# Kernel optimization log

Hardware: AMD Instinct MI355X
Metric: run time of the kernel (lower is better)

The kernel has to match this reference:

```python
import jax, jax.numpy as jnp
import numpy as np

N = 20000        # nodes
E = 320000       # edges
F_IN = 512       # feature_size
H = 512          # hidden_dim (z dim)
OUT = 1024       # output_size


def setup_inputs() -> dict:
    key = jax.random.key(0)
    ks = jax.random.split(key, 24)
    p = lambda k, shape: jax.random.normal(k, shape, jnp.float32) * 0.02
    return {
        "x": jax.random.normal(ks[0], (N, F_IN), jnp.float32),
        "edge_index": jax.random.randint(ks[1], (2, E), 0, N),
        "edge_weight": jax.random.uniform(ks[2], (E,), dtype=jnp.float32),
        "beta": jnp.float32(1.0),
        "y_target": jax.random.uniform(ks[3], (1,), dtype=jnp.float32),
        "eps": jax.random.normal(ks[4], (N, H), jnp.float32),
        # GCNConv weights (in_dim, out_dim) + bias
        "W1": p(ks[5], (F_IN, 1024)), "b1": jnp.zeros((1024,), jnp.float32),
        "W2": p(ks[6], (1024, 512)), "b2": jnp.zeros((512,), jnp.float32),
        "W3": p(ks[7], (512, 256)),  "b3": jnp.zeros((256,), jnp.float32),
        # VAE heads
        "Wmu": p(ks[8], (256, H)),  "bmu": jnp.zeros((H,), jnp.float32),
        "Wlv": p(ks[9], (256, H)),  "blv": jnp.zeros((H,), jnp.float32),
        # decoder MLP: (2H+1) -> (2H+1) -> OUT
        "Wd1": p(ks[10], (2 * H + 1, 2 * H + 1)), "bd1": jnp.zeros((2 * H + 1,), jnp.float32),
        "Wd2": p(ks[11], (2 * H + 1, OUT)),       "bd2": jnp.zeros((OUT,), jnp.float32),
    }


def gcn_conv(x, W, b, src, dst, ew):
    # PyG GCNConv: add self-loops (weight 1), symmetric deg normalization,
    # aggregate normalized neighbor messages of x @ W, then add bias.
    xw = x @ W                                             # [N, out]
    deg = jax.ops.segment_sum(ew, dst, num_segments=N) + 1.0
    dinv = jax.lax.rsqrt(deg)                              # [N]
    norm = dinv[src] * ew * dinv[dst]                      # [E]
    agg = jax.ops.segment_sum(norm[:, None] * xw[src], dst, num_segments=N)
    return agg + (dinv * dinv)[:, None] * xw + b


def l2norm(x):
    n = jnp.sqrt(jnp.sum(x * x, axis=1, keepdims=True))
    return x / jnp.maximum(n, 1e-12)


def reference(x, edge_index, edge_weight, beta, y_target, eps,
              W1, b1, W2, b2, W3, b3, Wmu, bmu, Wlv, blv, Wd1, bd1, Wd2, bd2):
    src, dst = edge_index[0], edge_index[1]
    h = jax.nn.relu(l2norm(gcn_conv(x, W1, b1, src, dst, edge_weight)))
    h = jax.nn.relu(l2norm(gcn_conv(h, W2, b2, src, dst, edge_weight)))
    h = jax.nn.relu(l2norm(gcn_conv(h, W3, b3, src, dst, edge_weight)))
    mu = h @ Wmu + bmu                                     # [N, H]
    logvar = h @ Wlv + blv                                 # [N, H]
    # reparameterize(mu, beta * logvar) with eps ~ 0.01 * N(0,1)
    std = jnp.exp(0.5 * beta * logvar)
    z = mu + (0.01 * eps) * std                            # [N, H]
    out1 = jnp.max(z, axis=0, keepdims=True)               # global max pool [1, H]
    out2 = jnp.mean(z, axis=0, keepdims=True)              # global mean pool [1, H]
    reduce_z = jnp.concatenate([out1, out2, y_target[:, None]], axis=-1)  # [1, 2H+1]
    hdec = jax.nn.relu(reduce_z @ Wd1 + bd1)
    recon_x = jax.nn.sigmoid(hdec @ Wd2 + bd2)             # [1, OUT]
    return (recon_x, mu, logvar)
```

## Files before the change

kernel.cpp:

```cpp
#include <hip/hip_runtime.h>

#define NN 20000
#define EE 320000
#define RCH 40
#define RPC 500
#define MPAD 20096
#define DKB 128
#define DCH 9

typedef unsigned short u16;
typedef unsigned int u32;
typedef __attribute__((ext_vector_type(8))) short short8;
typedef __attribute__((ext_vector_type(4))) float f32x4;

__device__ inline float bf16lo(u32 u) { return __uint_as_float(u << 16); }
__device__ inline float bf16hi(u32 u) { return __uint_as_float(u & 0xffff0000u); }
__device__ inline u16 f2b(float f) {
  u32 u = __float_as_uint(f);
  u += 0x7fffu + ((u >> 16) & 1u);
  return (u16)(u >> 16);
}
__device__ inline u32 pack2(float a, float b) {
  return (u32)f2b(a) | ((u32)f2b(b) << 16);
}

__device__ inline void gload16(const void* g, void* l) {
  __builtin_amdgcn_global_load_lds(
      (const __attribute__((address_space(1))) void*)g,
      (__attribute__((address_space(3))) void*)l, 16, 0, 0);
}

__global__ void k_zeroi(int* __restrict__ p, int n) {
  int i = blockIdx.x * blockDim.x + threadIdx.x;
  if (i < n) p[i] = 0;
}

__global__ void k_f2b2(const float* __restrict__ in, u16* __restrict__ out, int npairs) {
  for (int i = blockIdx.x * blockDim.x + threadIdx.x; i < npairs; i += gridDim.x * blockDim.x) {
    float2 v = *(const float2*)(in + 2 * i);
    ((u32*)out)[i] = pack2(v.x, v.y);
  }
}

__global__ void k_wt(const float* __restrict__ W, u16* __restrict__ WT, int K, int N) {
  int k = blockIdx.y * 256 + threadIdx.x;
  int n = blockIdx.x;
  WT[(size_t)n * K + k] = f2b(W[(size_t)k * N + n]);
}

__global__ void k_count(const int* __restrict__ ei, int* __restrict__ counts) {
  int e = blockIdx.x * blockDim.x + threadIdx.x;
  if (e < EE) atomicAdd(counts + ei[EE + e], 1);
}

__global__ __launch_bounds__(256)
void k_scan(const int* __restrict__ counts, int* __restrict__ rowptr, int* __restrict__ cursor) {
  const int CHUNK = (NN + 255) / 256;
  int t = threadIdx.x;
  int lo = t * CHUNK, hi = min(lo + CHUNK, NN);
  int s = 0;
  for (int i = lo; i < hi; ++i) s += counts[i];
  __shared__ int tsum[256];
  tsum[t] = s;
  __syncthreads();
  if (t == 0) {
    int run = 0;
    for (int i = 0; i < 256; ++i) { int v = tsum[i]; tsum[i] = run; run += v; }
  }
  __syncthreads();
  int run = tsum[t];
  for (int i = lo; i < hi; ++i) {
    rowptr[i] = run;
    cursor[i] = run;
    run += counts[i];
  }
  if (t == 255) rowptr[NN] = EE;
}

__global__ void k_fill(const int* __restrict__ ei, const float* __restrict__ ew,
                       int* __restrict__ cursor, int* __restrict__ colsrc,
                       float* __restrict__ ecw) {
  int e = blockIdx.x * blockDim.x + threadIdx.x;
  if (e < EE) {
    int d = ei[EE + e];
    int pos = atomicAdd(cursor + d, 1);
    colsrc[pos] = ei[e];
    ecw[pos] = ew[e];
  }
}

__global__ void k_degcsr(const int* __restrict__ rowptr, const float* __restrict__ ecw,
                         float* __restrict__ dinv, float* __restrict__ dinv2) {
  int i = blockIdx.x * blockDim.x + threadIdx.x;
  if (i < NN) {
    float s = 0.f;
    for (int e = rowptr[i]; e < rowptr[i + 1]; ++e) s += ecw[e];
    float d = s + 1.0f;
    dinv[i] = rsqrtf(d);
    dinv2[i] = 1.0f / d;
  }
}

template <bool STORE_BF16, bool HAS_BIAS>
__global__ __launch_bounds__(256)
void k_mfma(const u16* __restrict__ A, const u16* __restrict__ BT,
            const float* __restrict__ bias, void* __restrict__ C,
            int M, int K, int N) {
  __shared__ u16 Asm[128 * 32];
  __shared__ u16 Bsm[128 * 32];
  const int tid = threadIdx.x;
  const int m0 = blockIdx.x * 128;
  const int n0 = blockIdx.y * 128;
  const int lane = tid & 63;
  const int wave = tid >> 6;
  const int wm = (wave >> 1) * 64;
  const int wn = (wave & 1) * 64;
  const int qm = lane & 15;
  const int quad = lane >> 4;

  f32x4 acc[4][4];
#pragma unroll
  for (int i = 0; i < 4; ++i)
#pragma unroll
    for (int j = 0; j < 4; ++j) acc[i][j] = (f32x4){0.f, 0.f, 0.f, 0.f};

  for (int k0 = 0; k0 < K; k0 += 32) {
#pragma unroll
    for (int h = 0; h < 2; ++h) {
      int c = h * 256 + tid;
      int row = c >> 2, kc = c & 3;
      gload16(A + (size_t)(m0 + row) * K + k0 + kc * 8, Asm + c * 8);
      gload16(BT + (size_t)(n0 + row) * K + k0 + kc * 8, Bsm + c * 8);
    }
    __syncthreads();
    short8 af[4], bfr[4];
#pragma unroll
    for (int i = 0; i < 4; ++i)
      af[i] = *(const short8*)(Asm + (wm + i * 16 + qm) * 32 + quad * 8);
#pragma unroll
    for (int j = 0; j < 4; ++j)
      bfr[j] = *(const short8*)(Bsm + (wn + j * 16 + qm) * 32 + quad * 8);
#pragma unroll
    for (int i = 0; i < 4; ++i)
#pragma unroll
      for (int j = 0; j < 4; ++j)
        acc[i][j] = __builtin_amdgcn_mfma_f32_16x16x32_bf16(af[i], bfr[j], acc[i][j], 0, 0, 0);
    __syncthreads();
  }

#pragma unroll
  for (int i = 0; i < 4; ++i) {
#pragma unroll
    for (int r = 0; r < 4; ++r) {
      int row = m0 + wm + i * 16 + quad * 4 + r;
      if (row >= M) continue;
#pragma unroll
      for (int j = 0; j < 4; ++j) {
        int col = n0 + wn + j * 16 + qm;
        float v = acc[i][j][r];
        if (HAS_BIAS) v += bias[col];
        if (STORE_BF16) ((u16*)C)[(size_t)row * N + col] = f2b(v);
        else ((float*)C)[(size_t)row * N + col] = v;
      }
    }
  }
}

template <int NT, bool PRE>
__global__ __launch_bounds__(NT)
void k_gather(const int* __restrict__ rowptr, const int* __restrict__ colsrc,
              const float* __restrict__ ecw, const float* __restrict__ dinv,
              const float* __restrict__ dinv2, const u16* __restrict__ xw,
              const float* __restrict__ bias, u16* __restrict__ h) {
  const int O = 2 * NT;
  const int row = blockIdx.x;
  const int tid = threadIdx.x;
  const float dv = dinv[row], dv2 = dinv2[row];
  u32 u = ((const u32*)(xw + (size_t)row * O))[tid];
  float a0 = dv2 * bf16lo(u);
  float a1 = dv2 * bf16hi(u);
  if (!PRE) { a0 += bias[2 * tid]; a1 += bias[2 * tid + 1]; }

  __shared__ int s_src[NT];
  __shared__ float s_w[NT];
  const int e0 = rowptr[row], e1 = rowptr[row + 1];
  for (int base = e0; base < e1; base += NT) {
    int cnt = min(NT, e1 - base);
    __syncthreads();
    if (tid < cnt) {
      int s = colsrc[base + tid];
      s_src[tid] = s;
      s_w[tid] = dinv[s] * ecw[base + tid] * dv;
    }
    __syncthreads();
    for (int e = 0; e < cnt; ++e) {
      float w = s_w[e];
      u32 v = ((const u32*)(xw + (size_t)s_src[e] * O))[tid];
      a0 += w * bf16lo(v);
      a1 += w * bf16hi(v);
    }
  }

  if (PRE) {
    ((u32*)h)[(size_t)row * NT + tid] = pack2(a0, a1);
    return;
  }
  float ss = a0 * a0 + a1 * a1;
#pragma unroll
  for (int off = 32; off > 0; off >>= 1) ss += __shfl_down(ss, off, 64);
  __shared__ float red[NT / 64];
  __shared__ float s_scale;
  if ((tid & 63) == 0) red[tid >> 6] = ss;
  __syncthreads();
  if (tid == 0) {
    float t = 0.f;
#pragma unroll
    for (int i = 0; i < NT / 64; ++i) t += red[i];
    s_scale = 1.0f / fmaxf(sqrtf(t), 1e-12f);
  }
  __syncthreads();
  float sc = s_scale;
  ((u32*)h)[(size_t)row * NT + tid] = pack2(fmaxf(a0 * sc, 0.f), fmaxf(a1 * sc, 0.f));
}

__global__ __launch_bounds__(256)
void k_l2relu(const u16* __restrict__ t, u16* __restrict__ h) {
  const int row = blockIdx.x;
  const int tid = threadIdx.x;
  const u32* tr = (const u32*)(t + (size_t)row * 1024);
  u32 u0 = tr[tid], u1 = tr[256 + tid];
  float a0 = bf16lo(u0), a1 = bf16hi(u0), a2 = bf16lo(u1), a3 = bf16hi(u1);
  float ss = a0 * a0 + a1 * a1 + a2 * a2 + a3 * a3;
#pragma unroll
  for (int off = 32; off > 0; off >>= 1) ss += __shfl_down(ss, off, 64);
  __shared__ float red[4];
  __shared__ float s_scale;
  if ((tid & 63) == 0) red[tid >> 6] = ss;
  __syncthreads();
  if (tid == 0) {
    float s = red[0] + red[1] + red[2] + red[3];
    s_scale = 1.0f / fmaxf(sqrtf(s), 1e-12f);
  }
  __syncthreads();
  float sc = s_scale;
  u32* hr = (u32*)(h + (size_t)row * 1024);
  hr[tid]       = pack2(fmaxf(a0 * sc, 0.f), fmaxf(a1 * sc, 0.f));
  hr[256 + tid] = pack2(fmaxf(a2 * sc, 0.f), fmaxf(a3 * sc, 0.f));
}

__global__ void k_pool_partial(const float* __restrict__ mu, const float* __restrict__ lv,
                               const float* __restrict__ eps, const float* __restrict__ beta_p,
                               float* __restrict__ pmax, float* __restrict__ psum) {
  int tx = threadIdx.x, ty = threadIdx.y;
  int col = blockIdx.x * 64 + tx;
  int by = blockIdx.y;
  float beta = beta_p[0];
  float m = -3.4e38f, s = 0.f;
  for (int i = by * RPC + ty; i < (by + 1) * RPC; i += 4) {
    size_t idx = (size_t)i * 512 + col;
    float z = mu[idx] + 0.01f * eps[idx] * expf(0.5f * beta * lv[idx]);
    m = fmaxf(m, z);
    s += z;
  }
  __shared__ float sm[4][64], su[4][64];
  sm[ty][tx] = m; su[ty][tx] = s;
  __syncthreads();
  if (ty == 0) {
    m = fmaxf(fmaxf(sm[0][tx], sm[1][tx]), fmaxf(sm[2][tx], sm[3][tx]));
    s = su[0][tx] + su[1][tx] + su[2][tx] + su[3][tx];
    pmax[(size_t)by * 512 + col] = m;
    psum[(size_t)by * 512 + col] = s;
  }
}

__global__ void k_pool_combine(const float* __restrict__ pmax, const float* __restrict__ psum,
                               const float* __restrict__ yt, float* __restrict__ rz) {
  int col = threadIdx.x;
  float m = -3.4e38f, s = 0.f;
  for (int c = 0; c < RCH; ++c) {
    m = fmaxf(m, pmax[(size_t)c * 512 + col]);
    s += psum[(size_t)c * 512 + col];
  }
  rz[col] = m;
  rz[512 + col] = s / (float)NN;
  if (col == 0) rz[1024] = yt[0];
}

__global__ __launch_bounds__(256)
void k_dec_partial(const float* __restrict__ v, const float* __restrict__ W,
                   float* __restrict__ partial, int Kdim, int Ndim) {
  int b = blockIdx.x;
  int lo = b * DCH;
  float rv[DCH];
#pragma unroll
  for (int j = 0; j < DCH; ++j) rv[j] = (lo + j < Kdim) ? v[lo + j] : 0.f;
  for (int n = threadIdx.x; n < Ndim; n += 256) {
    float s = 0.f;
#pragma unroll
    for (int j = 0; j < DCH; ++j)
      if (lo + j < Kdim) s += rv[j] * W[(size_t)(lo + j) * Ndim + n];
    partial[(size_t)b * Ndim + n] = s;
  }
}

template <int ACT>
__global__ __launch_bounds__(256)
void k_dec_combine(const float* __restrict__ partial, const float* __restrict__ bias,
                   float* __restrict__ out, int Ndim) {
  int n = blockIdx.x * 256 + threadIdx.x;
  if (n >= Ndim) return;
  float s = bias[n];
  for (int b = 0; b < DKB; ++b) s += partial[(size_t)b * Ndim + n];
  out[n] = (ACT == 0) ? fmaxf(s, 0.f) : 1.0f / (1.0f + expf(-s));
}

extern "C" void kernel_launch(void* const* d_in, const int* in_sizes, int n_in,
                              void* d_out, int out_size, void* d_ws, size_t ws_size,
                              hipStream_t stream) {
  const float* x    = (const float*)d_in[0];
  const int*   ei   = (const int*)d_in[1];
  const float* ew   = (const float*)d_in[2];
  const float* beta = (const float*)d_in[3];
  const float* yt   = (const float*)d_in[4];
  const float* eps  = (const float*)d_in[5];
  const float* W1   = (const float*)d_in[6];  const float* b1  = (const float*)d_in[7];
  const float* W2   = (const float*)d_in[8];  const float* b2  = (const float*)d_in[9];
  const float* W3   = (const float*)d_in[10]; const float* b3  = (const float*)d_in[11];
  const float* Wmu  = (const float*)d_in[12]; const float* bmu = (const float*)d_in[13];
  const float* Wlv  = (const float*)d_in[14]; const float* blv = (const float*)d_in[15];
  const float* Wd1  = (const float*)d_in[16]; const float* bd1 = (const float*)d_in[17];
  const float* Wd2  = (const float*)d_in[18]; const float* bd2 = (const float*)d_in[19];

  char* wsb = (char*)d_ws;
  size_t off = 0;
  auto alloc_f = [&](size_t n) { float* p = (float*)(wsb + off); off += n * sizeof(float); return p; };
  auto alloc_i = [&](size_t n) { int* p = (int*)(wsb + off); off += n * sizeof(int); return p; };
  auto alloc_h = [&](size_t n) { u16* p = (u16*)(wsb + off); off += ((n * 2 + 3) & ~(size_t)3); return p; };

  int* counts  = alloc_i(NN);
  int* rowptr  = alloc_i(NN + 1);
  int* cursor  = alloc_i(NN);
  int* colsrc  = alloc_i(EE);
  float* ecw   = alloc_f(EE);
  float* dinv  = alloc_f(NN);
  float* din2  = alloc_f(NN);
  float* pmax  = alloc_f(RCH * 512);
  float* psum  = alloc_f(RCH * 512);
  float* rz    = alloc_f(1028);
  float* hdec  = alloc_f(1028);
  float* part1 = alloc_f((size_t)DKB * 1025);
  float* part2 = alloc_f((size_t)DKB * 1024);
  u16* W1T  = alloc_h(1024 * 512);
  u16* W2T  = alloc_h(512 * 1024);
  u16* W3T  = alloc_h(256 * 512);
  u16* WmuT = alloc_h(512 * 256);
  u16* WlvT = alloc_h(512 * 256);
  u16* xb   = alloc_h((size_t)MPAD * 512);
  u16* aggx = alloc_h((size_t)MPAD * 512);
  u16* bufT = alloc_h((size_t)MPAD * 1024);
  u16* bufH = alloc_h((size_t)MPAD * 1024);
  u16* h2   = alloc_h((size_t)MPAD * 512);
  u16* h3   = xb;
  u16* z2   = bufT;
  u16* z3   = bufH;

  float* out_f  = (float*)d_out;
  float* mu_out = out_f + 1024;
  float* lv_out = out_f + 1024 + (size_t)NN * 512;

  const int MT = (NN + 127) / 128;

  k_f2b2<<<4096, 256, 0, stream>>>(x, xb, NN * 512 / 2);
  k_wt<<<dim3(1024, 2), 256, 0, stream>>>(W1, W1T, 512, 1024);
  k_wt<<<dim3(512, 4), 256, 0, stream>>>(W2, W2T, 1024, 512);
  k_wt<<<dim3(256, 2), 256, 0, stream>>>(W3, W3T, 512, 256);
  k_wt<<<dim3(512, 1), 256, 0, stream>>>(Wmu, WmuT, 256, 512);
  k_wt<<<dim3(512, 1), 256, 0, stream>>>(Wlv, WlvT, 256, 512);

  k_zeroi<<<(NN + 255) / 256, 256, 0, stream>>>(counts, NN);
  k_count<<<(EE + 255) / 256, 256, 0, stream>>>(ei, counts);
  k_scan<<<1, 256, 0, stream>>>(counts, rowptr, cursor);
  k_fill<<<(EE + 255) / 256, 256, 0, stream>>>(ei, ew, cursor, colsrc, ecw);
  k_degcsr<<<(NN + 255) / 256, 256, 0, stream>>>(rowptr, ecw, dinv, din2);

  k_gather<256, true><<<NN, 256, 0, stream>>>(rowptr, colsrc, ecw, dinv, din2, xb, nullptr, aggx);
  k_mfma<true, true><<<dim3(MT, 8), 256, 0, stream>>>(aggx, W1T, b1, bufT, NN, 512, 1024);
  k_l2relu<<<NN, 256, 0, stream>>>(bufT, bufH);

  k_mfma<true, false><<<dim3(MT, 4), 256, 0, stream>>>(bufH, W2T, nullptr, z2, NN, 1024, 512);
  k_gather<256, false><<<NN, 256, 0, stream>>>(rowptr, colsrc, ecw, dinv, din2, z2, b2, h2);

  k_mfma<true, false><<<dim3(MT, 2), 256, 0, stream>>>(h2, W3T, nullptr, z3, NN, 512, 256);
  k_gather<128, false><<<NN, 128, 0, stream>>>(rowptr, colsrc, ecw, dinv, din2, z3, b3, h3);

  k_mfma<false, true><<<dim3(MT, 4), 256, 0, stream>>>(h3, WmuT, bmu, mu_out, NN, 256, 512);
  k_mfma<false, true><<<dim3(MT, 4), 256, 0, stream>>>(h3, WlvT, blv, lv_out, NN, 256, 512);

  k_pool_partial<<<dim3(8, RCH), dim3(64, 4), 0, stream>>>(mu_out, lv_out, eps, beta, pmax, psum);
  k_pool_combine<<<1, 512, 0, stream>>>(pmax, psum, yt, rz);

  k_dec_partial<<<DKB, 256, 0, stream>>>(rz, Wd1, part1, 1025, 1025);
  k_dec_combine<0><<<5, 256, 0, stream>>>(part1, bd1, hdec, 1025);
  k_dec_partial<<<DKB, 256, 0, stream>>>(hdec, Wd2, part2, 1025, 1024);
  k_dec_combine<1><<<4, 256, 0, stream>>>(part2, bd2, out_f, 1024);
}
```

Baseline: 732.4 us.

## Fuse mu/logvar head GEMMs with reparameterization and pooling partials

Replaces the two separate head GEMMs and the pooling partial kernel with one kernel that computes mu and logvar for the same tile, then the reparameterized z and per-tile column max and sum in the epilogue. This avoids re-reading the 2x20000x512 float outputs for pooling and shares the A-tile loads between both heads. The cost is double the accumulator registers (128 floats per thread), which may reduce occupancy, and a combine step over 157 tile partials instead of 40.

```diff
diff --git a/kernel.cpp b/kernel.cpp
--- a/kernel.cpp
+++ b/kernel.cpp
@@ -2,9 +2,8 @@
 
 #define NN 20000
 #define EE 320000
-#define RCH 40
-#define RPC 500
 #define MPAD 20096
+#define MTILES 157
 #define DKB 128
 #define DCH 9
 
@@ -166,6 +165,136 @@
   }
 }
 
+__global__ __launch_bounds__(256)
+void k_heads(const u16* __restrict__ A, const u16* __restrict__ BmuT,
+             const u16* __restrict__ BlvT, const float* __restrict__ bmu,
+             const float* __restrict__ blv, const float* __restrict__ eps,
+             const float* __restrict__ beta_p, float* __restrict__ mu_out,
+             float* __restrict__ lv_out, float* __restrict__ pmax,
+             float* __restrict__ psum) {
+  const int K = 256, N = 512;
+  __shared__ u16 Asm[128 * 32];
+  __shared__ u16 Bmu[128 * 32];
+  __shared__ u16 Blv[128 * 32];
+  __shared__ float smax[256], ssum[256];
+  const int tid = threadIdx.x;
+  const int m0 = blockIdx.x * 128;
+  const int n0 = blockIdx.y * 128;
+  const int lane = tid & 63;
+  const int wave = tid >> 6;
+  const int wm = (wave >> 1) * 64;
+  const int wn = (wave & 1) * 64;
+  const int qm = lane & 15;
+  const int quad = lane >> 4;
+
+  f32x4 am[4][4], al[4][4];
+#pragma unroll
+  for (int i = 0; i < 4; ++i)
+#pragma unroll
+    for (int j = 0; j < 4; ++j) {
+      am[i][j] = (f32x4){0.f, 0.f, 0.f, 0.f};
+      al[i][j] = (f32x4){0.f, 0.f, 0.f, 0.f};
+    }
+
+  for (int k0 = 0; k0 < K; k0 += 32) {
+#pragma unroll
+    for (int h = 0; h < 2; ++h) {
+      int c = h * 256 + tid;
+      int row = c >> 2, kc = c & 3;
+      gload16(A + (size_t)(m0 + row) * K + k0 + kc * 8, Asm + c * 8);
+      gload16(BmuT + (size_t)(n0 + row) * K + k0 + kc * 8, Bmu + c * 8);
+      gload16(BlvT + (size_t)(n0 + row) * K + k0 + kc * 8, Blv + c * 8);
+    }
+    __syncthreads();
+    short8 af[4], bm[4], bl[4];
+#pragma unroll
+    for (int i = 0; i < 4; ++i)
+      af[i] = *(const short8*)(Asm + (wm + i * 16 + qm) * 32 + quad * 8);
+#pragma unroll
+    for (int j = 0; j < 4; ++j) {
+      bm[j] = *(const short8*)(Bmu + (wn + j * 16 + qm) * 32 + quad * 8);
+      bl[j] = *(const short8*)(Blv + (wn + j * 16 + qm) * 32 + quad * 8);
+    }
+#pragma unroll
+    for (int i = 0; i < 4; ++i)
+#pragma unroll
+      for (int j = 0; j < 4; ++j) {
+        am[i][j] = __builtin_amdgcn_mfma_f32_16x16x32_bf16(af[i], bm[j], am[i][j], 0, 0, 0);
+        al[i][j] = __builtin_amdgcn_mfma_f32_16x16x32_bf16(af[i], bl[j], al[i][j], 0, 0, 0);
+      }
+    __syncthreads();
+  }
+
+  const float beta = beta_p[0];
+  float biasm[4], biasl[4];
+#pragma unroll
+  for (int j = 0; j < 4; ++j) {
+    int col = n0 + wn + j * 16 + qm;
+    biasm[j] = bmu[col];
+    biasl[j] = blv[col];
+  }
+  float zmax[4] = {-3.4e38f, -3.4e38f, -3.4e38f, -3.4e38f};
+  float zsum[4] = {0.f, 0.f, 0.f, 0.f};
+#pragma unroll
+  for (int i = 0; i < 4; ++i) {
+#pragma unroll
+    for (int r = 0; r < 4; ++r) {
+      int row = m0 + wm + i * 16 + quad * 4 + r;
+      if (row >= NN) continue;
+#pragma unroll
+      for (int j = 0; j < 4; ++j) {
+        int col = n0 + wn + j * 16 + qm;
+        float vm = am[i][j][r] + biasm[j];
+        float vl = al[i][j][r] + biasl[j];
+        size_t idx = (size_t)row * N + col;
+        mu_out[idx] = vm;
+        lv_out[idx] = vl;
+        float z = vm + 0.01f * eps[idx] * expf(0.5f * beta * vl);
+        zmax[j] = fmaxf(zmax[j], z);
+        zsum[j] += z;
+      }
+    }
+  }
+#pragma unroll
+  for (int j = 0; j < 4; ++j) {
+#pragma unroll
+    for (int off = 16; off <= 32; off <<= 1) {
+      zmax[j] = fmaxf(zmax[j], __shfl_xor(zmax[j], off, 64));
+      zsum[j] += __shfl_xor(zsum[j], off, 64);
+    }
+  }
+  if (quad == 0) {
+#pragma unroll
+    for (int j = 0; j < 4; ++j) {
+      smax[wave * 64 + j * 16 + qm] = zmax[j];
+      ssum[wave * 64 + j * 16 + qm] = zsum[j];
+    }
+  }
+  __syncthreads();
+  if (tid < 128) {
+    int cn = tid;
+    int w0 = (cn < 64) ? 0 : 1;
+    int c = cn & 63;
+    float m = fmaxf(smax[w0 * 64 + c], smax[(w0 + 2) * 64 + c]);
+    float s = ssum[w0 * 64 + c] + ssum[(w0 + 2) * 64 + c];
+    pmax[(size_t)blockIdx.x * N + n0 + cn] = m;
+    psum[(size_t)blockIdx.x * N + n0 + cn] = s;
+  }
+}
+
+__global__ void k_zred(const float* __restrict__ pmax, const float* __restrict__ psum,
+                       const float* __restrict__ yt, float* __restrict__ rz) {
+  int col = threadIdx.x;
+  float m = -3.4e38f, s = 0.f;
+  for (int c = 0; c < MTILES; ++c) {
+    m = fmaxf(m, pmax[(size_t)c * 512 + col]);
+    s += psum[(size_t)c * 512 + col];
+  }
+  rz[col] = m;
+  rz[512 + col] = s / (float)NN;
+  if (col == 0) rz[1024] = yt[0];
+}
+
 template <int NT, bool PRE>
 __global__ __launch_bounds__(NT)
 void k_gather(const int* __restrict__ rowptr, const int* __restrict__ colsrc,
@@ -246,44 +375,6 @@
   u32* hr = (u32*)(h + (size_t)row * 1024);
   hr[tid]       = pack2(fmaxf(a0 * sc, 0.f), fmaxf(a1 * sc, 0.f));
   hr[256 + tid] = pack2(fmaxf(a2 * sc, 0.f), fmaxf(a3 * sc, 0.f));
-}
-
-__global__ void k_pool_partial(const float* __restrict__ mu, const float* __restrict__ lv,
-                               const float* __restrict__ eps, const float* __restrict__ beta_p,
-                               float* __restrict__ pmax, float* __restrict__ psum) {
-  int tx = threadIdx.x, ty = threadIdx.y;
-  int col = blockIdx.x * 64 + tx;
-  int by = blockIdx.y;
-  float beta = beta_p[0];
-  float m = -3.4e38f, s = 0.f;
-  for (int i = by * RPC + ty; i < (by + 1) * RPC; i += 4) {
-    size_t idx = (size_t)i * 512 + col;
-    float z = mu[idx] + 0.01f * eps[idx] * expf(0.5f * beta * lv[idx]);
-    m = fmaxf(m, z);
-    s += z;
-  }
-  __shared__ float sm[4][64], su[4][64];
-  sm[ty][tx] = m; su[ty][tx] = s;
-  __syncthreads();
-  if (ty == 0) {
-    m = fmaxf(fmaxf(sm[0][tx], sm[1][tx]), fmaxf(sm[2][tx], sm[3][tx]));
-    s = su[0][tx] + su[1][tx] + su[2][tx] + su[3][tx];
-    pmax[(size_t)by * 512 + col] = m;
-    psum[(size_t)by * 512 + col] = s;
-  }
-}
-
-__global__ void k_pool_combine(const float* __restrict__ pmax, const float* __restrict__ psum,
-                               const float* __restrict__ yt, float* __restrict__ rz) {
-  int col = threadIdx.x;
-  float m = -3.4e38f, s = 0.f;
-  for (int c = 0; c < RCH; ++c) {
-    m = fmaxf(m, pmax[(size_t)c * 512 + col]);
-    s += psum[(size_t)c * 512 + col];
-  }
-  rz[col] = m;
-  rz[512 + col] = s / (float)NN;
-  if (col == 0) rz[1024] = yt[0];
 }
 
 __global__ __launch_bounds__(256)
@@ -344,8 +435,8 @@
   float* ecw   = alloc_f(EE);
   float* dinv  = alloc_f(NN);
   float* din2  = alloc_f(NN);
-  float* pmax  = alloc_f(RCH * 512);
-  float* psum  = alloc_f(RCH * 512);
+  float* pmax  = alloc_f((size_t)MTILES * 512);
+  float* psum  = alloc_f((size_t)MTILES * 512);
   float* rz    = alloc_f(1028);
   float* hdec  = alloc_f(1028);
   float* part1 = alloc_f((size_t)DKB * 1025);
@@ -368,7 +459,7 @@
   float* mu_out = out_f + 1024;
   float* lv_out = out_f + 1024 + (size_t)NN * 512;
 
-  const int MT = (NN + 127) / 128;
+  const int MT = MTILES;
 
   k_f2b2<<<4096, 256, 0, stream>>>(x, xb, NN * 512 / 2);
   k_wt<<<dim3(1024, 2), 256, 0, stream>>>(W1, W1T, 512, 1024);
@@ -393,11 +484,9 @@
   k_mfma<true, false><<<dim3(MT, 2), 256, 0, stream>>>(h2, W3T, nullptr, z3, NN, 512, 256);
   k_gather<128, false><<<NN, 128, 0, stream>>>(rowptr, colsrc, ecw, dinv, din2, z3, b3, h3);
 
-  k_mfma<false, true><<<dim3(MT, 4), 256, 0, stream>>>(h3, WmuT, bmu, mu_out, NN, 256, 512);
-  k_mfma<false, true><<<dim3(MT, 4), 256, 0, stream>>>(h3, WlvT, blv, lv_out, NN, 256, 512);
-
-  k_pool_partial<<<dim3(8, RCH), dim3(64, 4), 0, stream>>>(mu_out, lv_out, eps, beta, pmax, psum);
-  k_pool_combine<<<1, 512, 0, stream>>>(pmax, psum, yt, rz);
+  k_heads<<<dim3(MT, 4), 256, 0, stream>>>(h3, WmuT, WlvT, bmu, blv, eps, beta,
+                                           mu_out, lv_out, pmax, psum);
+  k_zred<<<1, 512, 0, stream>>>(pmax, psum, yt, rz);
 
   k_dec_partial<<<DKB, 256, 0, stream>>>(rz, Wd1, part1, 1025, 1025);
   k_dec_combine<0><<<5, 256, 0, stream>>>(part1, bd1, hdec, 1025);
```

Result: faster. 707.9 us (-3.3%).
